# Optimization experiments

Hardware: AMD Instinct MI355X
Metric: run time of the kernel (lower is better)

## Reference

```python
import jax, jax.numpy as jnp
import numpy as np

N, E, B, DIN, D = 65536, 1048576, 256, 32, 64
NUM_STEPS_MP = 2   # num_step_message_passing
SET2SET_STEPS = 3  # processing_steps
NUM_CLASSES = 4


def setup_inputs() -> dict:
    key = jax.random.key(0)
    ks = jax.random.split(key, 24)
    def gl(k, shape, fan_in):
        return (jax.random.normal(k, shape, jnp.float32) / np.sqrt(fan_in)).astype(jnp.float32)
    x = jax.random.normal(ks[0], (N, DIN), jnp.float32)
    edge_index = jax.random.randint(ks[1], (2, E), 0, N, dtype=jnp.int32).astype(jnp.int64)
    batch = jnp.sort(jax.random.randint(ks[2], (N,), 0, B, dtype=jnp.int32)).astype(jnp.int64)
    inp = dict(
        x=x, edge_index=edge_index, batch=batch,
        # conv1.mlp: Linear(DIN -> D)
        W_mlp=gl(ks[3], (D, DIN), DIN), b_mlp=jnp.zeros((D,), jnp.float32),
        # HenrionConv linear (D -> D), messages scatter-summed over edges
        W_conv=gl(ks[4], (D, D), D), b_conv=jnp.zeros((D,), jnp.float32),
        # GRU(input = D + DIN, hidden = D); gate order r,z,n (PyTorch)
        gru_W_ih=gl(ks[5], (3 * D, D + DIN), D + DIN),
        gru_W_hh=gl(ks[6], (3 * D, D), D),
        gru_b_ih=jnp.zeros((3 * D,), jnp.float32),
        gru_b_hh=jnp.zeros((3 * D,), jnp.float32),
        # Set2Set LSTM(input = 2D, hidden = D); gate order i,f,g,o (PyTorch)
        lstm_W_ih=gl(ks[7], (4 * D, 2 * D), 2 * D),
        lstm_W_hh=gl(ks[8], (4 * D, D), D),
        lstm_b_ih=jnp.zeros((4 * D,), jnp.float32),
        lstm_b_hh=jnp.zeros((4 * D,), jnp.float32),
        # head MLPs
        W1=gl(ks[9], (D, 2 * D), 2 * D), b1=jnp.zeros((D,), jnp.float32),
        W2=gl(ks[10], (NUM_CLASSES, D), D), b2=jnp.zeros((NUM_CLASSES,), jnp.float32),
        num_graphs=B,
    )
    return inp


def _forward(x, edge_index, batch, W_mlp, b_mlp, W_conv, b_conv,
             gru_W_ih, gru_W_hh, gru_b_ih, gru_b_hh,
             lstm_W_ih, lstm_W_hh, lstm_b_ih, lstm_b_hh,
             W1, b1, W2, b2, num_graphs):
    n = x.shape[0]
    d = W_mlp.shape[0]
    src, dst = edge_index[0], edge_index[1]

    # ---- Henrion_MPNNConv ----
    out = x @ W_mlp.T + b_mlp            # [N, D]
    h = out
    for _ in range(NUM_STEPS_MP):
        # HenrionConv: linear on source node features, scatter-sum to destinations
        msg = (out @ W_conv.T + b_conv)[src]               # [E, D] gather
        m = jax.ops.segment_sum(msg, dst, num_segments=n)  # [N, D] scatter
        inp = jnp.concatenate([m, x], axis=-1)             # [N, D+DIN]
        # GRU cell (seq len 1)
        gi = inp @ gru_W_ih.T + gru_b_ih
        gh = h @ gru_W_hh.T + gru_b_hh
        gi_r, gi_z, gi_n = jnp.split(gi, 3, axis=-1)
        gh_r, gh_z, gh_n = jnp.split(gh, 3, axis=-1)
        r = jax.nn.sigmoid(gi_r + gh_r)
        z = jax.nn.sigmoid(gi_z + gh_z)
        ng = jnp.tanh(gi_n + r * gh_n)
        h = (1.0 - z) * ng + z * h
        out = h

    # ---- Set2Set (processing_steps = 3) ----
    bsz = num_graphs
    q_star = jnp.zeros((bsz, 2 * d), out.dtype)
    hl = jnp.zeros((bsz, d), out.dtype)
    cl = jnp.zeros((bsz, d), out.dtype)
    for _ in range(SET2SET_STEPS):
        gates = q_star @ lstm_W_ih.T + lstm_b_ih + hl @ lstm_W_hh.T + lstm_b_hh
        gi, gf, gg, go = jnp.split(gates, 4, axis=-1)
        cl = jax.nn.sigmoid(gf) * cl + jax.nn.sigmoid(gi) * jnp.tanh(gg)
        hl = jax.nn.sigmoid(go) * jnp.tanh(cl)
        q = hl                                             # [B, D]
        e = jnp.sum(out * q[batch], axis=-1)               # [N]
        e_max = jax.ops.segment_max(e, batch, num_segments=bsz)
        e_max = jnp.where(jnp.isfinite(e_max), e_max, 0.0)
        a = jnp.exp(e - e_max[batch])
        a_sum = jax.ops.segment_sum(a, batch, num_segments=bsz)
        a = a / jnp.maximum(a_sum[batch], 1e-16)           # segment softmax
        r = jax.ops.segment_sum(a[:, None] * out, batch, num_segments=bsz)  # [B, D]
        q_star = jnp.concatenate([q, r], axis=-1)          # [B, 2D]

    # ---- head (eval mode: dropout is identity) ----
    hid = jax.nn.relu(q_star @ W1.T + b1)
    logits = hid @ W2.T + b2
    return jax.nn.log_softmax(logits, axis=-1)             # [B, 4]


def reference(x, edge_index, batch, W_mlp, b_mlp, W_conv, b_conv,
              gru_W_ih, gru_W_hh, gru_b_ih, gru_b_hh,
              lstm_W_ih, lstm_W_hh, lstm_b_ih, lstm_b_hh,
              W1, b1, W2, b2, num_graphs):
    return _forward(x, edge_index, batch, W_mlp, b_mlp, W_conv, b_conv,
                    gru_W_ih, gru_W_hh, gru_b_ih, gru_b_hh,
                    lstm_W_ih, lstm_W_hh, lstm_b_ih, lstm_b_hh,
                    W1, b1, W2, b2, num_graphs)
```

## Files before the change

kernel.cpp:

```cpp
#include <hip/hip_runtime.h>
#include <math.h>

constexpr int Nn  = 65536;
constexpr int Ne  = 1048576;
constexpr int Bg  = 256;
constexpr int DIN = 32;
constexpr int D   = 64;

constexpr int NB   = 256;
constexpr int BCAP = 6144;

typedef __attribute__((ext_vector_type(8))) short bf16x8;
typedef __attribute__((ext_vector_type(8))) unsigned short u16x8;
typedef __attribute__((ext_vector_type(4))) float f32x4;

__device__ __forceinline__ float sigf(float x) { return 1.0f / (1.0f + expf(-x)); }

__device__ __forceinline__ unsigned short bf16_rne(float f) {
  unsigned u = __float_as_uint(f);
  unsigned r = u + 0x7FFFu + ((u >> 16) & 1u);
  return (unsigned short)(r >> 16);
}
__device__ __forceinline__ float bf16_tof(unsigned short h) {
  return __uint_as_float(((unsigned)h) << 16);
}
__device__ __forceinline__ void split2(float f, unsigned short& hi, unsigned short& lo) {
  hi = bf16_rne(f);
  lo = bf16_rne(f - bf16_tof(hi));
}
__device__ __forceinline__ float recon(unsigned short hi, unsigned short lo) {
  return bf16_tof(hi) + bf16_tof(lo);
}

#define MFMA(a, b, c) __builtin_amdgcn_mfma_f32_16x16x32_bf16(a, b, c, 0, 0, 0)

__global__ void k_prepw(const float* __restrict__ W_mlp, const float* __restrict__ W_conv,
                        const float* __restrict__ gWih, const float* __restrict__ gWhh,
                        const float* __restrict__ b_conv,
                        const float* __restrict__ lW_ih, const float* __restrict__ lW_hh,
                        const float* __restrict__ W1,
                        unsigned short* __restrict__ mlp_h, unsigned short* __restrict__ mlp_l,
                        unsigned short* __restrict__ gw_h,  unsigned short* __restrict__ gw_l,
                        float* __restrict__ WihT, float* __restrict__ WhhT,
                        float* __restrict__ W1T, float* __restrict__ vfold,
                        const int* __restrict__ batch, int* __restrict__ gp,
                        int* __restrict__ rp) {
  int idx = blockIdx.x * 256 + threadIdx.x;
  if (idx < 30720) {
    int c = idx / 6144, rem = idx % 6144;
    int nt = rem >> 9, lane = (rem >> 3) & 63, j = rem & 7;
    int n = nt * 16 + (lane & 15);
    int kk = c * 32 + (lane >> 4) * 8 + j;
    float v;
    if (c < 2) {
      float s = 0.f;
      for (int o = 0; o < 64; ++o) s = fmaf(gWih[n * 96 + o], W_conv[o * 64 + kk], s);
      v = s;
    } else if (c == 2) {
      v = gWih[n * 96 + kk];
    } else {
      v = gWhh[n * 64 + (c - 3) * 32 + (lane >> 4) * 8 + j];
    }
    unsigned short hi, lo; split2(v, hi, lo);
    gw_h[idx] = hi; gw_l[idx] = lo;
    return;
  }
  if (idx < 32768) {
    int lp = idx - 30720;
    int nt = lp >> 9, lane = (lp >> 3) & 63, j = lp & 7;
    int n = nt * 16 + (lane & 15);
    unsigned short hi, lo;
    split2(W_mlp[n * 32 + (lane >> 4) * 8 + j], hi, lo);
    mlp_h[lp] = hi; mlp_l[lp] = lo;
    return;
  }
  int t = idx - 32768;
  if (t < 32768) {
    int row = t / 128, k = t % 128;
    WihT[k * 256 + row] = lW_ih[t];
  } else if (t < 49152) {
    int j = t - 32768;
    int row = j / 64, k = j % 64;
    WhhT[k * 256 + row] = lW_hh[j];
  } else if (t < 57344) {
    int j = t - 49152;
    int row = j / 128, k = j % 128;
    W1T[k * 64 + row] = W1[j];
  } else if (t < 57344 + Bg + 1) {
    int g = t - 57344;
    if (g == 0) rp[Nn] = Ne;
    int lo = 0, hi = Nn;
    while (lo < hi) {
      int mid = (lo + hi) >> 1;
      if (batch[mid] < g) lo = mid + 1; else hi = mid;
    }
    gp[g] = lo;
  } else if (t < 57344 + 257 + 192) {
    int g = t - 57344 - 257;
    float s = 0.f;
    for (int o = 0; o < 64; ++o) s = fmaf(gWih[g * 96 + o], b_conv[o], s);
    vfold[g] = s;
  }
}

__global__ __launch_bounds__(256) void k_conv1(const float* __restrict__ x,
                                               const unsigned short* __restrict__ Wh,
                                               const unsigned short* __restrict__ Wl,
                                               const float* __restrict__ bias,
                                               unsigned short* __restrict__ hph,
                                               unsigned short* __restrict__ hpl,
                                               unsigned short* __restrict__ Aih,
                                               unsigned short* __restrict__ Ail) {
  int wave = threadIdx.x >> 6, lane = threadIdx.x & 63;
  int quad = lane >> 4;
  int n0w = blockIdx.x * 64 + wave * 16;
  int rowA = n0w + (lane & 15);
  const float4* xp = (const float4*)&x[(size_t)rowA * 32 + quad * 8];
  float4 xa = xp[0], xb = xp[1];
  float xv[8] = {xa.x, xa.y, xa.z, xa.w, xb.x, xb.y, xb.z, xb.w};
  bf16x8 ah, al;
#pragma unroll
  for (int j = 0; j < 8; ++j) {
    unsigned short hi, lo; split2(xv[j], hi, lo);
    ah[j] = (short)hi; al[j] = (short)lo;
  }
  *(bf16x8*)&Aih[(size_t)rowA * 96 + 64 + quad * 8] = ah;
  *(bf16x8*)&Ail[(size_t)rowA * 96 + 64 + quad * 8] = al;

  f32x4 acc[4] = {};
#pragma unroll
  for (int nt = 0; nt < 4; ++nt) {
    bf16x8 bh = *(const bf16x8*)&Wh[(nt * 64 + lane) * 8];
    bf16x8 bl = *(const bf16x8*)&Wl[(nt * 64 + lane) * 8];
    acc[nt] = MFMA(ah, bh, acc[nt]);
    acc[nt] = MFMA(ah, bl, acc[nt]);
    acc[nt] = MFMA(al, bh, acc[nt]);
  }
  int col0 = lane & 15;
#pragma unroll
  for (int nt = 0; nt < 4; ++nt) {
    float bv = bias[nt * 16 + col0];
#pragma unroll
    for (int r = 0; r < 4; ++r) {
      int node = n0w + quad * 4 + r;
      float v = acc[nt][r] + bv;
      size_t o = (size_t)node * 64 + nt * 16 + col0;
      unsigned short hi, lo; split2(v, hi, lo);
      hph[o] = hi; hpl[o] = lo;
    }
  }
}

__global__ __launch_bounds__(256, 2) void k_gru(const unsigned short* __restrict__ Aih,
                                                const unsigned short* __restrict__ Ail,
                                                const unsigned short* __restrict__ Hh,
                                                const unsigned short* __restrict__ Hl,
                                                const unsigned short* __restrict__ gw_h,
                                                const unsigned short* __restrict__ gw_l,
                                                const float* __restrict__ b_ih,
                                                const float* __restrict__ b_hh,
                                                const float* __restrict__ vfold,
                                                const int* __restrict__ rp,
                                                const int* __restrict__ srcs,
                                                unsigned short* __restrict__ nph,
                                                unsigned short* __restrict__ npl) {
  __shared__ unsigned short sW[2][12288];
  int tid = threadIdx.x;
  int wave = tid >> 6, lane = tid & 63;
  int quad = lane >> 4;
  int n0w = blockIdx.x * 128 + wave * 32;
  int rowA0 = n0w + (lane & 15);

  bf16x8 fh[2][2], fl[2][2];
  const size_t q8 = (size_t)(quad * 8);
#pragma unroll
  for (int tile = 0; tile < 2; ++tile) {
    int row = rowA0 + tile * 16;
    int s = rp[row], e = rp[row + 1];
    int n = e - s;
    const int* sp = srcs + s;
    float acc0[8] = {}, acc1[8] = {};
    int i = 0;
    for (; i + 4 <= n; i += 4) {
      int s0 = sp[i], s1 = sp[i + 1], s2 = sp[i + 2], s3 = sp[i + 3];
      u16x8 a0 = *(const u16x8*)&Hh[(size_t)s0 * 64 + q8];
      u16x8 b0 = *(const u16x8*)&Hh[(size_t)s0 * 64 + 32 + q8];
      u16x8 a1 = *(const u16x8*)&Hh[(size_t)s1 * 64 + q8];
      u16x8 b1 = *(const u16x8*)&Hh[(size_t)s1 * 64 + 32 + q8];
      u16x8 a2 = *(const u16x8*)&Hh[(size_t)s2 * 64 + q8];
      u16x8 b2 = *(const u16x8*)&Hh[(size_t)s2 * 64 + 32 + q8];
      u16x8 a3 = *(const u16x8*)&Hh[(size_t)s3 * 64 + q8];
      u16x8 b3 = *(const u16x8*)&Hh[(size_t)s3 * 64 + 32 + q8];
#pragma unroll
      for (int j = 0; j < 8; ++j) {
        acc0[j] += bf16_tof(a0[j]);
        acc1[j] += bf16_tof(b0[j]);
      }
#pragma unroll
      for (int j = 0; j < 8; ++j) {
        acc0[j] += bf16_tof(a1[j]);
        acc1[j] += bf16_tof(b1[j]);
      }
#pragma unroll
      for (int j = 0; j < 8; ++j) {
        acc0[j] += bf16_tof(a2[j]);
        acc1[j] += bf16_tof(b2[j]);
      }
#pragma unroll
      for (int j = 0; j < 8; ++j) {
        acc0[j] += bf16_tof(a3[j]);
        acc1[j] += bf16_tof(b3[j]);
      }
    }
    for (; i < n; ++i) {
      int src = sp[i];
      u16x8 v0 = *(const u16x8*)&Hh[(size_t)src * 64 + q8];
      u16x8 v1 = *(const u16x8*)&Hh[(size_t)src * 64 + 32 + q8];
#pragma unroll
      for (int j = 0; j < 8; ++j) {
        acc0[j] += bf16_tof(v0[j]);
        acc1[j] += bf16_tof(v1[j]);
      }
    }
#pragma unroll
    for (int j = 0; j < 8; ++j) {
      unsigned short hi, lo;
      split2(acc0[j], hi, lo);
      fh[tile][0][j] = (short)hi; fl[tile][0][j] = (short)lo;
      split2(acc1[j], hi, lo);
      fh[tile][1][j] = (short)hi; fl[tile][1][j] = (short)lo;
    }
  }

  f32x4 acc0[12] = {}, acc1[12] = {};
  f32x4 aN0[4] = {}, aN1[4] = {};

  bf16x8 gvh[3], gvl[3];
#pragma unroll
  for (int j = 0; j < 3; ++j) {
    gvh[j] = *(const bf16x8*)&gw_h[(tid + j * 256) * 8];
    gvl[j] = *(const bf16x8*)&gw_l[(tid + j * 256) * 8];
  }
#pragma unroll
  for (int j = 0; j < 3; ++j) {
    *(bf16x8*)&sW[0][(tid + j * 256) * 8] = gvh[j];
    *(bf16x8*)&sW[0][6144 + (tid + j * 256) * 8] = gvl[j];
  }
  __syncthreads();

#pragma unroll
  for (int c = 0; c < 5; ++c) {
    const int buf = c & 1;
    if (c < 4) {
#pragma unroll
      for (int j = 0; j < 3; ++j) {
        gvh[j] = *(const bf16x8*)&gw_h[(c + 1) * 6144 + (tid + j * 256) * 8];
        gvl[j] = *(const bf16x8*)&gw_l[(c + 1) * 6144 + (tid + j * 256) * 8];
      }
    }
    bf16x8 a0h, a0l, a1h, a1l;
    if (c < 2) {
      a0h = fh[0][c]; a0l = fl[0][c];
      a1h = fh[1][c]; a1l = fl[1][c];
    } else if (c == 2) {
      size_t b0 = (size_t)rowA0 * 96 + 64 + quad * 8;
      size_t b1 = (size_t)(rowA0 + 16) * 96 + 64 + quad * 8;
      a0h = *(const bf16x8*)&Aih[b0]; a0l = *(const bf16x8*)&Ail[b0];
      a1h = *(const bf16x8*)&Aih[b1]; a1l = *(const bf16x8*)&Ail[b1];
    } else {
      size_t b0 = (size_t)rowA0 * 64 + (c - 3) * 32 + quad * 8;
      size_t b1 = (size_t)(rowA0 + 16) * 64 + (c - 3) * 32 + quad * 8;
      a0h = *(const bf16x8*)&Hh[b0]; a0l = *(const bf16x8*)&Hl[b0];
      a1h = *(const bf16x8*)&Hh[b1]; a1l = *(const bf16x8*)&Hl[b1];
    }
    const unsigned short* sw = sW[buf];
#pragma unroll
    for (int nt = 0; nt < 12; ++nt) {
      bf16x8 bh = *(const bf16x8*)&sw[(nt * 64 + lane) * 8];
      bf16x8 bl = *(const bf16x8*)&sw[6144 + (nt * 64 + lane) * 8];
      if (c < 3 || nt < 8) {
        acc0[nt] = MFMA(a0h, bh, acc0[nt]);
        acc0[nt] = MFMA(a0h, bl, acc0[nt]);
        acc0[nt] = MFMA(a0l, bh, acc0[nt]);
        acc1[nt] = MFMA(a1h, bh, acc1[nt]);
        acc1[nt] = MFMA(a1h, bl, acc1[nt]);
        acc1[nt] = MFMA(a1l, bh, acc1[nt]);
      } else {
        aN0[nt - 8] = MFMA(a0h, bh, aN0[nt - 8]);
        aN0[nt - 8] = MFMA(a0h, bl, aN0[nt - 8]);
        aN0[nt - 8] = MFMA(a0l, bh, aN0[nt - 8]);
        aN1[nt - 8] = MFMA(a1h, bh, aN1[nt - 8]);
        aN1[nt - 8] = MFMA(a1h, bl, aN1[nt - 8]);
        aN1[nt - 8] = MFMA(a1l, bh, aN1[nt - 8]);
      }
    }
    if (c < 4) {
#pragma unroll
      for (int j = 0; j < 3; ++j) {
        *(bf16x8*)&sW[1 - buf][(tid + j * 256) * 8] = gvh[j];
        *(bf16x8*)&sW[1 - buf][6144 + (tid + j * 256) * 8] = gvl[j];
      }
    }
    __syncthreads();
  }

  int col0 = lane & 15;
#pragma unroll
  for (int tile = 0; tile < 2; ++tile) {
    int nb = n0w + tile * 16;
#pragma unroll
    for (int r = 0; r < 4; ++r) {
      int node = nb + quad * 4 + r;
      float degf = (float)(rp[node + 1] - rp[node]);
#pragma unroll
      for (int nt = 0; nt < 4; ++nt) {
        int g = nt * 16 + col0;
        size_t o = (size_t)node * 64 + g;
        float br  = b_ih[g] + b_hh[g] + degf * vfold[g];
        float bz  = b_ih[64 + g] + b_hh[64 + g] + degf * vfold[64 + g];
        float bin = b_ih[128 + g] + degf * vfold[128 + g];
        float bhn = b_hh[128 + g];
        float gr = tile ? acc1[nt][r]     : acc0[nt][r];
        float gz = tile ? acc1[nt + 4][r] : acc0[nt + 4][r];
        float gn = tile ? acc1[nt + 8][r] : acc0[nt + 8][r];
        float hn = tile ? aN1[nt][r]      : aN0[nt][r];
        float rr = sigf(gr + br);
        float zz = sigf(gz + bz);
        float nn = tanhf(gn + bin + rr * (hn + bhn));
        float h_old = recon(Hh[o], Hl[o]);
        float hv = (1.f - zz) * nn + zz * h_old;
        unsigned short hi, lo; split2(hv, hi, lo);
        nph[o] = hi; npl[o] = lo;
      }
    }
  }
}

__global__ __launch_bounds__(256) void k_bucket(const int* __restrict__ eidx,
                                                int* __restrict__ gcur,
                                                int* __restrict__ payload) {
  __shared__ int lcnt[NB];
  __shared__ int lcur[NB];
  int t = threadIdx.x;
  int e0 = blockIdx.x * 4096;
  lcnt[t] = 0;
  __syncthreads();
  int ds[16], ss[16];
#pragma unroll
  for (int i = 0; i < 16; ++i) {
    int e = e0 + i * 256 + t;
    ds[i] = eidx[Ne + e];
    ss[i] = eidx[e];
    atomicAdd(&lcnt[ds[i] >> 8], 1);
  }
  __syncthreads();
  lcur[t] = atomicAdd(&gcur[t * 16], lcnt[t]);
  __syncthreads();
#pragma unroll
  for (int i = 0; i < 16; ++i) {
    int b = ds[i] >> 8;
    int p = atomicAdd(&lcur[b], 1);
    if (p < BCAP) payload[b * BCAP + p] = (ss[i] << 8) | (ds[i] & 255);
  }
}

__global__ __launch_bounds__(256) void k_placeB(const int* __restrict__ gcur,
                                                const int* __restrict__ payload,
                                                int* __restrict__ rp,
                                                int* __restrict__ srcs) {
  __shared__ int sAll[NB];
  __shared__ int hst[NB];
  __shared__ int cur[NB];
  int b = blockIdx.x, t = threadIdx.x;
  sAll[t] = gcur[t * 16];
  hst[t] = 0;
  __syncthreads();
  int cnt = min(sAll[b], BCAP);
  for (int off = 1; off < NB; off <<= 1) {
    int v = (t >= off) ? sAll[t - off] : 0;
    __syncthreads();
    sAll[t] += v;
    __syncthreads();
  }
  int base = sAll[b] - gcur[b * 16];
  const int* pay = &payload[b * BCAP];
  for (int i = t; i < cnt; i += 256) atomicAdd(&hst[pay[i] & 255], 1);
  __syncthreads();
  int c = hst[t];
  cur[t] = c;
  __syncthreads();
  for (int off = 1; off < NB; off <<= 1) {
    int v = (t >= off) ? cur[t - off] : 0;
    __syncthreads();
    cur[t] += v;
    __syncthreads();
  }
  int excl = cur[t] - c;
  rp[b * 256 + t] = base + excl;
  cur[t] = base + excl;
  __syncthreads();
  for (int i = t; i < cnt; i += 256) {
    int pl = pay[i];
    int p = atomicAdd(&cur[pl & 255], 1);
    srcs[p] = pl >> 8;
  }
}

constexpr int LCAP = 448;
constexpr int LPAD = 68;
constexpr int S2T  = 512;
__global__ __launch_bounds__(S2T) void k_s2s(const unsigned short* __restrict__ hph,
                                             const unsigned short* __restrict__ hpl,
                                             const int* __restrict__ gp,
                                             const float* __restrict__ WihT,
                                             const float* __restrict__ WhhT,
                                             const float* __restrict__ b_ih,
                                             const float* __restrict__ b_hh,
                                             const float* __restrict__ W1T,
                                             const float* __restrict__ b1,
                                             const float* __restrict__ W2,
                                             const float* __restrict__ b2,
                                             float* __restrict__ outp) {
  extern __shared__ float hL[];
  int g = blockIdx.x;
  int t = threadIdx.x;
  int w = t >> 6, lane = t & 63;
  __shared__ float qstar_s[128];
  __shared__ float hs[64], cs[64], gates[256];
  __shared__ float eL[LCAP];
  __shared__ float partial[8][64];
  __shared__ float asum_p[8];
  __shared__ float l4[4];
  __shared__ float hid[64];

  if (t < 128) qstar_s[t] = 0.f;
  if (t < 64) { hs[t] = 0.f; cs[t] = 0.f; }
  int s = gp[g], e = gp[g + 1];
  int cnt = e - s;

  {
    int total = cnt * 64;
    for (int j = t * 4; j < total; j += S2T * 4) {
      int nd = j >> 6, col = j & 63;
      ushort4 hh = *(const ushort4*)&hph[(size_t)s * 64 + j];
      ushort4 ll = *(const ushort4*)&hpl[(size_t)s * 64 + j];
      float4 v;
      v.x = recon(hh.x, ll.x); v.y = recon(hh.y, ll.y);
      v.z = recon(hh.z, ll.z); v.w = recon(hh.w, ll.w);
      *(float4*)&hL[nd * LPAD + col] = v;
    }
  }

  for (int it = 0; it < 3; ++it) {
    __syncthreads();

    if (t < 256) {
      float acc = b_ih[t] + b_hh[t];
      for (int k = 0; k < 128; ++k) acc = fmaf(WihT[k * 256 + t], qstar_s[k], acc);
      for (int k = 0; k < 64; ++k)  acc = fmaf(WhhT[k * 256 + t], hs[k], acc);
      gates[t] = acc;
    }
    __syncthreads();
    if (t < 64) {
      float ig = sigf(gates[t]),        fg = sigf(gates[64 + t]);
      float gg = tanhf(gates[128 + t]), og = sigf(gates[192 + t]);
      float c = fg * cs[t] + ig * gg;
      float q = og * tanhf(c);
      cs[t] = c;
      hs[t] = q;
      qstar_s[t] = q;
    }
    __syncthreads();

    int c4 = (lane & 15) * 4;
    float4 qv = {qstar_s[c4], qstar_s[c4 + 1], qstar_s[c4 + 2], qstar_s[c4 + 3]};
    for (int i0 = s + w * 4; i0 < e; i0 += 32) {
      int node = i0 + (lane >> 4);
      float p = 0.f;
      if (node < e) {
        float4 hv = *(const float4*)&hL[(node - s) * LPAD + c4];
        p = hv.x * qv.x + hv.y * qv.y + hv.z * qv.z + hv.w * qv.w;
      }
      p += __shfl_xor(p, 1); p += __shfl_xor(p, 2);
      p += __shfl_xor(p, 4); p += __shfl_xor(p, 8);
      if (node < e && (lane & 15) == 0) eL[node - s] = p;
    }
    __syncthreads();

    float m = -INFINITY;
    for (int i = lane; i < cnt; i += 64) m = fmaxf(m, eL[i]);
#pragma unroll
    for (int o = 32; o >= 1; o >>= 1) m = fmaxf(m, __shfl_xor(m, o));
    float emax = isfinite(m) ? m : 0.f;

    float acc = 0.f, asum = 0.f;
    for (int i = s + w; i < e; i += 8) {
      float a = expf(eL[i - s] - emax);
      asum += a;
      acc = fmaf(a, hL[(i - s) * LPAD + lane], acc);
    }
    partial[w][lane] = acc;
    if (lane == 0) asum_p[w] = asum;
    __syncthreads();
    if (t < 64) {
      float r = 0.f, as = 0.f;
      for (int q = 0; q < 8; ++q) { r += partial[q][t]; as += asum_p[q]; }
      float rv = (cnt > 0) ? r / fmaxf(as, 1e-16f) : 0.f;
      qstar_s[64 + t] = rv;
    }
  }
  __syncthreads();

  if (t < 64) {
    float a1 = b1[t];
    for (int k = 0; k < 64; ++k)   a1 = fmaf(W1T[k * 64 + t], qstar_s[k], a1);
    for (int k = 64; k < 128; ++k) a1 = fmaf(W1T[k * 64 + t], qstar_s[k], a1);
    hid[t] = fmaxf(a1, 0.f);
  }
  __syncthreads();
  if (t < 4) {
    float lg = b2[t];
    for (int d = 0; d < 64; ++d) lg = fmaf(W2[t * 64 + d], hid[d], lg);
    l4[t] = lg;
  }
  __syncthreads();
  if (t < 4) {
    float mx = fmaxf(fmaxf(l4[0], l4[1]), fmaxf(l4[2], l4[3]));
    float ssum = expf(l4[0] - mx) + expf(l4[1] - mx) + expf(l4[2] - mx) + expf(l4[3] - mx);
    outp[g * 4 + t] = l4[t] - mx - logf(ssum);
  }
}

extern "C" void kernel_launch(void* const* d_in, const int* in_sizes, int n_in,
                              void* d_out, int out_size, void* d_ws, size_t ws_size,
                              hipStream_t stream) {
  const float* x        = (const float*)d_in[0];
  const int*   eidx     = (const int*)d_in[1];
  const int*   batch    = (const int*)d_in[2];
  const float* W_mlp    = (const float*)d_in[3];
  const float* b_mlp    = (const float*)d_in[4];
  const float* W_conv   = (const float*)d_in[5];
  const float* b_conv   = (const float*)d_in[6];
  const float* gW_ih    = (const float*)d_in[7];
  const float* gW_hh    = (const float*)d_in[8];
  const float* gb_ih    = (const float*)d_in[9];
  const float* gb_hh    = (const float*)d_in[10];
  const float* lW_ih    = (const float*)d_in[11];
  const float* lW_hh    = (const float*)d_in[12];
  const float* lb_ih    = (const float*)d_in[13];
  const float* lb_hh    = (const float*)d_in[14];
  const float* W1       = (const float*)d_in[15];
  const float* b1       = (const float*)d_in[16];
  const float* W2       = (const float*)d_in[17];
  const float* b2       = (const float*)d_in[18];
  float* outp = (float*)d_out;

  char* ws = (char*)d_ws;
  size_t off = 0;
  auto alloc = [&](size_t bytes) { size_t r = off; off = (off + bytes + 255) & ~(size_t)255; return r; };
  unsigned short* hpAh = (unsigned short*)(ws + alloc((size_t)Nn * 64 * 2));
  unsigned short* hpAl = (unsigned short*)(ws + alloc((size_t)Nn * 64 * 2));
  unsigned short* hpBh = (unsigned short*)(ws + alloc((size_t)Nn * 64 * 2));
  unsigned short* hpBl = (unsigned short*)(ws + alloc((size_t)Nn * 64 * 2));
  unsigned short* Aih  = (unsigned short*)(ws + alloc((size_t)Nn * 96 * 2));
  unsigned short* Ail  = (unsigned short*)(ws + alloc((size_t)Nn * 96 * 2));
  int*   rp    = (int*)(ws + alloc((size_t)(Nn + 1) * 4));
  int*   srcs  = (int*)(ws + alloc((size_t)Ne * 4));
  int*   gcur  = (int*)(ws + alloc((size_t)NB * 16 * 4));
  int*   payload = (int*)(ws + alloc((size_t)NB * BCAP * 4));
  int*   gp    = (int*)(ws + alloc((size_t)(Bg + 1) * 4));
  float* WihT  = (float*)(ws + alloc((size_t)128 * 256 * 4));
  float* WhhT  = (float*)(ws + alloc((size_t)64 * 256 * 4));
  float* W1T   = (float*)(ws + alloc((size_t)128 * 64 * 4));
  float* vfold = (float*)(ws + alloc(192 * 4));
  unsigned short* mlp_h = (unsigned short*)(ws + alloc(2048 * 2));
  unsigned short* mlp_l = (unsigned short*)(ws + alloc(2048 * 2));
  unsigned short* gw_h  = (unsigned short*)(ws + alloc(30720 * 2));
  unsigned short* gw_l  = (unsigned short*)(ws + alloc(30720 * 2));
  (void)in_sizes; (void)n_in; (void)out_size; (void)ws_size;

  hipMemsetAsync(gcur, 0, (size_t)NB * 16 * 4, stream);

  k_bucket<<<Ne / 4096, 256, 0, stream>>>(eidx, gcur, payload);
  k_placeB<<<NB, 256, 0, stream>>>(gcur, payload, rp, srcs);
  k_prepw<<<355, 256, 0, stream>>>(W_mlp, W_conv, gW_ih, gW_hh, b_conv,
                                   lW_ih, lW_hh, W1,
                                   mlp_h, mlp_l, gw_h, gw_l,
                                   WihT, WhhT, W1T, vfold, batch, gp, rp);

  k_conv1<<<Nn / 64, 256, 0, stream>>>(x, mlp_h, mlp_l, b_mlp, hpAh, hpAl, Aih, Ail);

  unsigned short *cph = hpAh, *cpl = hpAl, *nph = hpBh, *npl = hpBl;
  for (int step = 0; step < 2; ++step) {
    k_gru<<<Nn / 128, 256, 0, stream>>>(Aih, Ail, cph, cpl, gw_h, gw_l,
                                        gb_ih, gb_hh, vfold, rp, srcs, nph, npl);
    unsigned short* tu;
    tu = cph; cph = nph; nph = tu;
    tu = cpl; cpl = npl; npl = tu;
  }

  const size_t dynLds = (size_t)LCAP * LPAD * sizeof(float);
  static bool attr_set = false;
  if (!attr_set) {
    hipFuncSetAttribute((const void*)k_s2s,
                        hipFuncAttributeMaxDynamicSharedMemorySize,
                        (int)dynLds);
    attr_set = true;
  }
  k_s2s<<<Bg, S2T, dynLds, stream>>>(cph, cpl, gp, WihT, WhhT,
                                     lb_ih, lb_hh, W1T, b1, W2, b2, outp);
}
```

Before: 291.2 us.

## Use 512-thread GRU blocks with one 16-row tile per wave

The GRU kernel now runs 8 waves per block, each handling a single 16-node tile instead of two. This halves the per-thread accumulator and fragment registers and raises the launch-bounds occupancy target, giving more waves to hide latency on the irregular neighbor gathers. In exchange, each LDS weight chunk is reused by half as many rows per wave, and the larger block adds barrier overhead.

```diff
diff --git a/kernel.cpp b/kernel.cpp
--- a/kernel.cpp
+++ b/kernel.cpp
@@ -151,7 +151,7 @@
   }
 }
 
-__global__ __launch_bounds__(256, 2) void k_gru(const unsigned short* __restrict__ Aih,
+__global__ __launch_bounds__(512, 4) void k_gru(const unsigned short* __restrict__ Aih,
                                                 const unsigned short* __restrict__ Ail,
                                                 const unsigned short* __restrict__ Hh,
                                                 const unsigned short* __restrict__ Hl,
@@ -168,15 +168,12 @@
   int tid = threadIdx.x;
   int wave = tid >> 6, lane = tid & 63;
   int quad = lane >> 4;
-  int n0w = blockIdx.x * 128 + wave * 32;
-  int rowA0 = n0w + (lane & 15);
-
-  bf16x8 fh[2][2], fl[2][2];
+  int rowA = blockIdx.x * 128 + wave * 16 + (lane & 15);
+
+  bf16x8 fh[2], fl[2];
   const size_t q8 = (size_t)(quad * 8);
-#pragma unroll
-  for (int tile = 0; tile < 2; ++tile) {
-    int row = rowA0 + tile * 16;
-    int s = rp[row], e = rp[row + 1];
+  {
+    int s = rp[rowA], e = rp[rowA + 1];
     int n = e - s;
     const int* sp = srcs + s;
     float acc0[8] = {}, acc1[8] = {};
@@ -226,25 +223,28 @@
     for (int j = 0; j < 8; ++j) {
       unsigned short hi, lo;
       split2(acc0[j], hi, lo);
-      fh[tile][0][j] = (short)hi; fl[tile][0][j] = (short)lo;
+      fh[0][j] = (short)hi; fl[0][j] = (short)lo;
       split2(acc1[j], hi, lo);
-      fh[tile][1][j] = (short)hi; fl[tile][1][j] = (short)lo;
-    }
-  }
-
-  f32x4 acc0[12] = {}, acc1[12] = {};
-  f32x4 aN0[4] = {}, aN1[4] = {};
-
-  bf16x8 gvh[3], gvl[3];
-#pragma unroll
-  for (int j = 0; j < 3; ++j) {
-    gvh[j] = *(const bf16x8*)&gw_h[(tid + j * 256) * 8];
-    gvl[j] = *(const bf16x8*)&gw_l[(tid + j * 256) * 8];
-  }
-#pragma unroll
-  for (int j = 0; j < 3; ++j) {
-    *(bf16x8*)&sW[0][(tid + j * 256) * 8] = gvh[j];
-    *(bf16x8*)&sW[0][6144 + (tid + j * 256) * 8] = gvl[j];
+      fh[1][j] = (short)hi; fl[1][j] = (short)lo;
+    }
+  }
+
+  f32x4 acc[12] = {};
+  f32x4 aN[4] = {};
+
+  bf16x8 gvh0, gvl0, gvh1, gvl1;
+  const bool two = (tid < 256);
+  gvh0 = *(const bf16x8*)&gw_h[tid * 8];
+  gvl0 = *(const bf16x8*)&gw_l[tid * 8];
+  if (two) {
+    gvh1 = *(const bf16x8*)&gw_h[(tid + 512) * 8];
+    gvl1 = *(const bf16x8*)&gw_l[(tid + 512) * 8];
+  }
+  *(bf16x8*)&sW[0][tid * 8] = gvh0;
+  *(bf16x8*)&sW[0][6144 + tid * 8] = gvl0;
+  if (two) {
+    *(bf16x8*)&sW[0][(tid + 512) * 8] = gvh1;
+    *(bf16x8*)&sW[0][6144 + (tid + 512) * 8] = gvl1;
   }
   __syncthreads();
 
@@ -252,26 +252,22 @@
   for (int c = 0; c < 5; ++c) {
     const int buf = c & 1;
     if (c < 4) {
-#pragma unroll
-      for (int j = 0; j < 3; ++j) {
-        gvh[j] = *(const bf16x8*)&gw_h[(c + 1) * 6144 + (tid + j * 256) * 8];
-        gvl[j] = *(const bf16x8*)&gw_l[(c + 1) * 6144 + (tid + j * 256) * 8];
-      }
-    }
-    bf16x8 a0h, a0l, a1h, a1l;
+      gvh0 = *(const bf16x8*)&gw_h[(c + 1) * 6144 + tid * 8];
+      gvl0 = *(const bf16x8*)&gw_l[(c + 1) * 6144 + tid * 8];
+      if (two) {
+        gvh1 = *(const bf16x8*)&gw_h[(c + 1) * 6144 + (tid + 512) * 8];
+        gvl1 = *(const bf16x8*)&gw_l[(c + 1) * 6144 + (tid + 512) * 8];
+      }
+    }
+    bf16x8 ah, al;
     if (c < 2) {
-      a0h = fh[0][c]; a0l = fl[0][c];
-      a1h = fh[1][c]; a1l = fl[1][c];
+      ah = fh[c]; al = fl[c];
     } else if (c == 2) {
-      size_t b0 = (size_t)rowA0 * 96 + 64 + quad * 8;
-      size_t b1 = (size_t)(rowA0 + 16) * 96 + 64 + quad * 8;
-      a0h = *(const bf16x8*)&Aih[b0]; a0l = *(const bf16x8*)&Ail[b0];
-      a1h = *(const bf16x8*)&Aih[b1]; a1l = *(const bf16x8*)&Ail[b1];
+      size_t b0 = (size_t)rowA * 96 + 64 + quad * 8;
+      ah = *(const bf16x8*)&Aih[b0]; al = *(const bf16x8*)&Ail[b0];
     } else {
-      size_t b0 = (size_t)rowA0 * 64 + (c - 3) * 32 + quad * 8;
-      size_t b1 = (size_t)(rowA0 + 16) * 64 + (c - 3) * 32 + quad * 8;
-      a0h = *(const bf16x8*)&Hh[b0]; a0l = *(const bf16x8*)&Hl[b0];
-      a1h = *(const bf16x8*)&Hh[b1]; a1l = *(const bf16x8*)&Hl[b1];
+      size_t b0 = (size_t)rowA * 64 + (c - 3) * 32 + quad * 8;
+      ah = *(const bf16x8*)&Hh[b0]; al = *(const bf16x8*)&Hl[b0];
     }
     const unsigned short* sw = sW[buf];
 #pragma unroll
@@ -279,59 +275,51 @@
       bf16x8 bh = *(const bf16x8*)&sw[(nt * 64 + lane) * 8];
       bf16x8 bl = *(const bf16x8*)&sw[6144 + (nt * 64 + lane) * 8];
       if (c < 3 || nt < 8) {
-        acc0[nt] = MFMA(a0h, bh, acc0[nt]);
-        acc0[nt] = MFMA(a0h, bl, acc0[nt]);
-        acc0[nt] = MFMA(a0l, bh, acc0[nt]);
-        acc1[nt] = MFMA(a1h, bh, acc1[nt]);
-        acc1[nt] = MFMA(a1h, bl, acc1[nt]);
-        acc1[nt] = MFMA(a1l, bh, acc1[nt]);
+        acc[nt] = MFMA(ah, bh, acc[nt]);
+        acc[nt] = MFMA(ah, bl, acc[nt]);
+        acc[nt] = MFMA(al, bh, acc[nt]);
       } else {
-        aN0[nt - 8] = MFMA(a0h, bh, aN0[nt - 8]);
-        aN0[nt - 8] = MFMA(a0h, bl, aN0[nt - 8]);
-        aN0[nt - 8] = MFMA(a0l, bh, aN0[nt - 8]);
-        aN1[nt - 8] = MFMA(a1h, bh, aN1[nt - 8]);
-        aN1[nt - 8] = MFMA(a1h, bl, aN1[nt - 8]);
-        aN1[nt - 8] = MFMA(a1l, bh, aN1[nt - 8]);
+        aN[nt - 8] = MFMA(ah, bh, aN[nt - 8]);
+        aN[nt - 8] = MFMA(ah, bl, aN[nt - 8]);
+        aN[nt - 8] = MFMA(al, bh, aN[nt - 8]);
       }
     }
     if (c < 4) {
-#pragma unroll
-      for (int j = 0; j < 3; ++j) {
-        *(bf16x8*)&sW[1 - buf][(tid + j * 256) * 8] = gvh[j];
-        *(bf16x8*)&sW[1 - buf][6144 + (tid + j * 256) * 8] = gvl[j];
+      *(bf16x8*)&sW[1 - buf][tid * 8] = gvh0;
+      *(bf16x8*)&sW[1 - buf][6144 + tid * 8] = gvl0;
+      if (two) {
+        *(bf16x8*)&sW[1 - buf][(tid + 512) * 8] = gvh1;
+        *(bf16x8*)&sW[1 - buf][6144 + (tid + 512) * 8] = gvl1;
       }
     }
     __syncthreads();
   }
 
   int col0 = lane & 15;
-#pragma unroll
-  for (int tile = 0; tile < 2; ++tile) {
-    int nb = n0w + tile * 16;
-#pragma unroll
-    for (int r = 0; r < 4; ++r) {
-      int node = nb + quad * 4 + r;
-      float degf = (float)(rp[node + 1] - rp[node]);
-#pragma unroll
-      for (int nt = 0; nt < 4; ++nt) {
-        int g = nt * 16 + col0;
-        size_t o = (size_t)node * 64 + g;
-        float br  = b_ih[g] + b_hh[g] + degf * vfold[g];
-        float bz  = b_ih[64 + g] + b_hh[64 + g] + degf * vfold[64 + g];
-        float bin = b_ih[128 + g] + degf * vfold[128 + g];
-        float bhn = b_hh[128 + g];
-        float gr = tile ? acc1[nt][r]     : acc0[nt][r];
-        float gz = tile ? acc1[nt + 4][r] : acc0[nt + 4][r];
-        float gn = tile ? acc1[nt + 8][r] : acc0[nt + 8][r];
-        float hn = tile ? aN1[nt][r]      : aN0[nt][r];
-        float rr = sigf(gr + br);
-        float zz = sigf(gz + bz);
-        float nn = tanhf(gn + bin + rr * (hn + bhn));
-        float h_old = recon(Hh[o], Hl[o]);
-        float hv = (1.f - zz) * nn + zz * h_old;
-        unsigned short hi, lo; split2(hv, hi, lo);
-        nph[o] = hi; npl[o] = lo;
-      }
+  int nb = blockIdx.x * 128 + wave * 16;
+#pragma unroll
+  for (int r = 0; r < 4; ++r) {
+    int node = nb + quad * 4 + r;
+    float degf = (float)(rp[node + 1] - rp[node]);
+#pragma unroll
+    for (int nt = 0; nt < 4; ++nt) {
+      int g = nt * 16 + col0;
+      size_t o = (size_t)node * 64 + g;
+      float br  = b_ih[g] + b_hh[g] + degf * vfold[g];
+      float bz  = b_ih[64 + g] + b_hh[64 + g] + degf * vfold[64 + g];
+      float bin = b_ih[128 + g] + degf * vfold[128 + g];
+      float bhn = b_hh[128 + g];
+      float gr = acc[nt][r];
+      float gz = acc[nt + 4][r];
+      float gn = acc[nt + 8][r];
+      float hn = aN[nt][r];
+      float rr = sigf(gr + br);
+      float zz = sigf(gz + bz);
+      float nn = tanhf(gn + bin + rr * (hn + bhn));
+      float h_old = recon(Hh[o], Hl[o]);
+      float hv = (1.f - zz) * nn + zz * h_old;
+      unsigned short hi, lo; split2(hv, hi, lo);
+      nph[o] = hi; npl[o] = lo;
     }
   }
 }
@@ -592,7 +580,7 @@
 
   unsigned short *cph = hpAh, *cpl = hpAl, *nph = hpBh, *npl = hpBl;
   for (int step = 0; step < 2; ++step) {
-    k_gru<<<Nn / 128, 256, 0, stream>>>(Aih, Ail, cph, cpl, gw_h, gw_l,
+    k_gru<<<Nn / 128, 512, 0, stream>>>(Aih, Ail, cph, cpl, gw_h, gw_l,
                                         gb_ih, gb_hh, vfold, rp, srcs, nph, npl);
     unsigned short* tu;
     tu = cph; cph = nph; nph = tu;
```

Result: faster. 277.2 us (-4.8%).
